# Performance work log

Hardware: AMD Instinct MI355X
Metric: run time of the kernel (lower is better)

## Reference

```python
import jax, jax.numpy as jnp
import numpy as np

DIM = 256
HEADS = 8
KS = 3          # deform conv kernel size
N = KS * KS     # sampling points per output pixel
PAD = 1


def conv2d(x, w, b=None, stride=1, padding=0):
    out = jax.lax.conv_general_dilated(
        x, w, (stride, stride), [(padding, padding)] * 2,
        dimension_numbers=('NCHW', 'OIHW', 'NCHW'))
    if b is not None:
        out = out + b[None, :, None, None]
    return out


def deform_conv(x, w_pconv, b_pconv, w_dconv):
    b, c, h, w = x.shape
    offset = conv2d(x, w_pconv, b_pconv, padding=1)      # (b, 2N, h, w)
    off = offset.transpose(0, 2, 3, 1)                   # (b, h, w, 2N); [:N]=x-off, [N:]=y-off
    xp = jnp.pad(x, ((0, 0), (0, 0), (PAD, PAD), (PAD, PAD)))
    hp, wp = h + 2 * PAD, w + 2 * PAD
    r = jnp.arange(-(KS - 1) // 2, (KS - 1) // 2 + 1, dtype=x.dtype)
    pnx, pny = jnp.meshgrid(r, r, indexing='ij')
    # sampling positions, 1-indexed into the padded input (matches the torch ref)
    px = off[..., :N] + pnx.reshape(-1) + jnp.arange(1, h + 1, dtype=x.dtype)[None, :, None, None]
    py = off[..., N:] + pny.reshape(-1) + jnp.arange(1, w + 1, dtype=x.dtype)[None, None, :, None]
    fx = jnp.floor(px)
    fy = jnp.floor(py)
    qlt_x = jnp.clip(fx, 0, hp - 1)
    qlt_y = jnp.clip(fy, 0, wp - 1)
    qrb_x = jnp.clip(fx + 1, 0, hp - 1)
    qrb_y = jnp.clip(fy + 1, 0, wp - 1)
    pxc = jnp.clip(px, 0, hp - 1)
    pyc = jnp.clip(py, 0, wp - 1)
    # bilinear weights (can be negative at clamped borders, as in the torch ref)
    g_lt = (1 + (qlt_x - pxc)) * (1 + (qlt_y - pyc))
    g_rb = (1 - (qrb_x - pxc)) * (1 - (qrb_y - pyc))
    g_lb = (1 + (qlt_x - pxc)) * (1 - (qrb_y - pyc))
    g_rt = (1 - (qrb_x - pxc)) * (1 + (qlt_y - pyc))
    ilt_x = qlt_x.astype(jnp.int32)
    ilt_y = qlt_y.astype(jnp.int32)
    irb_x = qrb_x.astype(jnp.int32)
    irb_y = qrb_y.astype(jnp.int32)

    def gather(xb, ix, iy):
        return xb[:, ix, iy]                              # (c, h, w, N)

    gat = jax.vmap(gather)
    x_lt = gat(xp, ilt_x, ilt_y)
    x_rb = gat(xp, irb_x, irb_y)
    x_lb = gat(xp, ilt_x, irb_y)
    x_rt = gat(xp, irb_x, ilt_y)
    x_off = (g_lt[:, None] * x_lt + g_rb[:, None] * x_rb
             + g_lb[:, None] * x_lb + g_rt[:, None] * x_rt)   # (b, c, h, w, N)
    # 'b c h w (i j) -> b c (h i) (w j)' then ks-strided conv
    x_off = x_off.reshape(b, c, h, w, KS, KS).transpose(0, 1, 2, 4, 3, 5)
    x_off = x_off.reshape(b, c, h * KS, w * KS)
    return conv2d(x_off, w_dconv, None, stride=KS)


def ssa_forward(x, w_pconv, b_pconv, w_dconv, w_qkv, temperature, w_proj):
    b, c, h, w = x.shape
    hw = h * w
    ch = c // HEADS
    q = deform_conv(x, w_pconv, b_pconv, w_dconv)         # (b, c, h, w)
    qkv = jnp.einsum('bchw,oc->bohw', x, w_qkv)           # 1x1 conv, (b, 3c, h, w)
    k = qkv[:, c:2 * c]
    v = qkv[:, 2 * c:]
    q = q.reshape(b, HEADS, ch, hw)
    k = k.reshape(b, HEADS, ch, hw)
    v = v.reshape(b, HEADS, ch, hw)
    k = k / jnp.maximum(jnp.linalg.norm(k, axis=-1, keepdims=True), 1e-12)
    v = v / jnp.maximum(jnp.linalg.norm(v, axis=-1, keepdims=True), 1e-12)
    attn = jnp.einsum('bhcn,bhdn->bhcd', q, k) * temperature[None]   # (b, h, ch, ch)
    attn = jax.nn.softmax(attn, axis=-1)
    out = jnp.einsum('bhcd,bhdn->bhcn', attn, v).reshape(b, c, h, w)
    return jnp.einsum('bchw,oc->bohw', out, w_proj)       # project_out 1x1


def setup_inputs() -> dict:
    key = jax.random.key(0)
    ks = jax.random.split(key, 6)
    B, H, W = 2, 96, 96
    x = jax.random.normal(ks[0], (B, DIM, H, W), jnp.float32)
    w_pconv = jax.random.normal(ks[1], (2 * N, DIM, KS, KS), jnp.float32) * 0.01
    b_pconv = jax.random.normal(ks[2], (2 * N,), jnp.float32) * 0.01
    w_dconv = jax.random.normal(ks[3], (DIM, DIM, KS, KS), jnp.float32) * 0.02
    w_qkv = jax.random.normal(ks[4], (3 * DIM, DIM), jnp.float32) * 0.05
    temperature = jnp.ones((HEADS, 1, 1), jnp.float32)
    w_proj = jax.random.normal(ks[5], (DIM, DIM), jnp.float32) * 0.05
    return dict(x=x, w_pconv=w_pconv, b_pconv=b_pconv, w_dconv=w_dconv,
                w_qkv=w_qkv, temperature=temperature, w_proj=w_proj)


def reference(x, w_pconv, b_pconv, w_dconv, w_qkv, temperature, w_proj):
    return ssa_forward(x, w_pconv, b_pconv, w_dconv, w_qkv, temperature, w_proj)
```

## Files before the change

### kernel.cpp

```cpp
#include <hip/hip_runtime.h>
#include <math.h>

#define BB 2
#define CC 256
#define HW 96
#define PP 9216
#define KO 18
#define HEADS 8
#define NCH 36

typedef short bf16x8 __attribute__((ext_vector_type(8)));
typedef float f32x4 __attribute__((ext_vector_type(4)));

#define NP_O    0UL
#define IDX_O   331776UL
#define WGT_O   995328UL
#define WT2_O   1658880UL
#define WP2_O   2248704UL
#define WQ2_O   2322432UL
#define W2_O    2453504UL
#define QP_O    2584576UL
#define KV_O    12021760UL
#define INV_O   21458944UL
#define AP_O    21459968UL
#define AT_O    22049792UL

__device__ __forceinline__ ushort f2bf_rne(float f) {
    unsigned u = __float_as_uint(f);
    unsigned r = (u + 0x7FFFu + ((u >> 16) & 1u)) >> 16;
    return (ushort)r;
}
__device__ __forceinline__ float bf2f(ushort h) {
    return __uint_as_float(((unsigned)h) << 16);
}

__global__ __launch_bounds__(256) void k_prep_wt(const float* __restrict__ wd,
                                                 ushort* __restrict__ h,
                                                 ushort* __restrict__ lo) {
    int tid = blockIdx.x * 256 + threadIdx.x;
    if (tid >= 9 * 8 * 1024 * 8) return;
    int e = tid & 7;
    int u = (tid >> 3) & 1023;
    int cs = (tid >> 13) & 7;
    int kk = tid >> 16;
    int oh = u >> 6, rem = u & 63;
    int lrow = rem & 15, lhi = rem >> 4;
    int o = oh * 16 + lrow;
    int c = cs * 32 + lhi * 8 + e;
    float v = wd[o * 2304 + c * 9 + kk];
    ushort hh = f2bf_rne(v);
    h[tid] = hh;
    lo[tid] = f2bf_rne(v - bf2f(hh));
}

__global__ __launch_bounds__(256) void k_prep_wp(const float* __restrict__ wp,
                                                 ushort* __restrict__ h,
                                                 ushort* __restrict__ lo) {
    int tid = blockIdx.x * 256 + threadIdx.x;
    if (tid >= 9 * 8 * 128 * 8) return;
    int e = tid & 7;
    int u = (tid >> 3) & 127;
    int cs = (tid >> 10) & 7;
    int kk = tid >> 13;
    int mf = u >> 6, rem = u & 63;
    int lrow = rem & 15, lhi = rem >> 4;
    int o = mf * 16 + lrow;
    int c = cs * 32 + lhi * 8 + e;
    float v = (o < KO) ? wp[(o * 256 + c) * 9 + kk] : 0.f;
    ushort hh = f2bf_rne(v);
    h[tid] = hh;
    lo[tid] = f2bf_rne(v - bf2f(hh));
}

__global__ __launch_bounds__(256) void k_prep_w(const float* __restrict__ W,
                                                ushort* __restrict__ h,
                                                ushort* __restrict__ lo,
                                                int total) {
    int tid = blockIdx.x * 256 + threadIdx.x;
    if (tid >= total) return;
    int e = tid & 7;
    int u = (tid >> 3) & 1023;
    int csg = (tid >> 13) & 7;
    int mt = tid >> 16;
    int rem = u & 63;
    int lrow = rem & 15, lhi = rem >> 4;
    int o = mt * 256 + (u >> 6) * 16 + lrow;
    int c = csg * 32 + lhi * 8 + e;
    float v = W[o * 256 + c];
    ushort hh = f2bf_rne(v);
    h[tid] = hh;
    lo[tid] = f2bf_rne(v - bf2f(hh));
}

__global__ __launch_bounds__(256) void k_pconv(const float* __restrict__ x,
                                               const ushort* __restrict__ wp2h,
                                               const ushort* __restrict__ wp2l,
                                               float* __restrict__ ppart) {
    int s = blockIdx.x;
    int xcd = s & 7;
    int b = xcd & 1, ks = xcd >> 1;
    int p0 = (s >> 3) * 64;
    int t = threadIdx.x;
    int l = t & 63, w = t >> 6;
    int lrow = l & 15, lhi = l >> 4;
    int p = t & 63, cg = t >> 6;
    __shared__ __align__(16) ushort Sh[64 * 40];
    __shared__ __align__(16) ushort Sl[64 * 40];
    f32x4 acc[2];
    acc[0] = (f32x4)0.f; acc[1] = (f32x4)0.f;
    const float* xb = x + (size_t)b * CC * PP;
    int pix = p0 + p;
    int i_ = pix / 96, j_ = pix % 96;
#pragma unroll 1
    for (int cs = 0; cs < 2; ++cs) {
        int csg = ks * 2 + cs;
        const float* xc0 = xb + (size_t)(csg * 32 + cg * 8) * PP;
#pragma unroll 1
        for (int kk = 0; kk < 9; ++kk) {
            int di = kk / 3 - 1, dj = kk % 3 - 1;
            bool vOK = ((unsigned)(i_ + di) < 96u) && ((unsigned)(j_ + dj) < 96u);
            int poff = pix + di * 96 + dj;
            __syncthreads();
            bf16x8 ah[2], al[2];
#pragma unroll
            for (int mf = 0; mf < 2; ++mf) {
                size_t gi = (((size_t)(kk * 8 + csg)) * 128 + (mf * 64 + l)) * 8;
                ah[mf] = *(const bf16x8*)&wp2h[gi];
                al[mf] = *(const bf16x8*)&wp2l[gi];
            }
            bf16x8 vh, vl;
#pragma unroll
            for (int i = 0; i < 8; ++i) {
                float v = vOK ? xc0[(size_t)i * PP + poff] : 0.f;
                ushort hh = f2bf_rne(v);
                vh[i] = (short)hh;
                vl[i] = (short)f2bf_rne(v - bf2f(hh));
            }
            *(bf16x8*)&Sh[p * 40 + cg * 8] = vh;
            *(bf16x8*)&Sl[p * 40 + cg * 8] = vl;
            __syncthreads();
            bf16x8 Bh = *(const bf16x8*)&Sh[(w * 16 + lrow) * 40 + lhi * 8];
            bf16x8 Bl = *(const bf16x8*)&Sl[(w * 16 + lrow) * 40 + lhi * 8];
#pragma unroll
            for (int mf = 0; mf < 2; ++mf) {
                acc[mf] = __builtin_amdgcn_mfma_f32_16x16x32_bf16(ah[mf], Bh, acc[mf], 0, 0, 0);
                acc[mf] = __builtin_amdgcn_mfma_f32_16x16x32_bf16(ah[mf], Bl, acc[mf], 0, 0, 0);
                acc[mf] = __builtin_amdgcn_mfma_f32_16x16x32_bf16(al[mf], Bh, acc[mf], 0, 0, 0);
            }
        }
    }
    float* pr = ppart + ((size_t)(ks * BB + b) * 32) * PP;
#pragma unroll
    for (int mf = 0; mf < 2; ++mf)
#pragma unroll
        for (int j = 0; j < 4; ++j)
            pr[(size_t)(mf * 16 + lhi * 4 + j) * PP + p0 + w * 16 + lrow] = acc[mf][j];
}

__global__ __launch_bounds__(256) void k_bilin2(const float* __restrict__ pp,
                                                const float* __restrict__ bp,
                                                int4* __restrict__ idx4,
                                                float4* __restrict__ wgt4) {
    int idx = blockIdx.x * 256 + threadIdx.x;
    if (idx >= BB * 9 * PP) return;
    int p = idx % PP;
    int bn = idx / PP;
    int n = bn % 9, b = bn / 9;
    int i = p / 96, j = p % 96;
    float ox = bp[n], oy = bp[n + 9];
#pragma unroll
    for (int k = 0; k < 4; ++k) {
        ox += pp[((size_t)(k * BB + b) * 32 + n) * PP + p];
        oy += pp[((size_t)(k * BB + b) * 32 + n + 9) * PP + p];
    }
    float px = ox + (float)(n / 3 - 1) + (float)(i + 1);
    float py = oy + (float)(n % 3 - 1) + (float)(j + 1);
    float fx = floorf(px), fy = floorf(py);
    float qltx = fminf(fmaxf(fx, 0.f), 97.f);
    float qlty = fminf(fmaxf(fy, 0.f), 97.f);
    float qrbx = fminf(fmaxf(fx + 1.f, 0.f), 97.f);
    float qrby = fminf(fmaxf(fy + 1.f, 0.f), 97.f);
    float pxc = fminf(fmaxf(px, 0.f), 97.f);
    float pyc = fminf(fmaxf(py, 0.f), 97.f);
    float glt = (1.f + (qltx - pxc)) * (1.f + (qlty - pyc));
    float grb = (1.f - (qrbx - pxc)) * (1.f - (qrby - pyc));
    float glb = (1.f + (qltx - pxc)) * (1.f - (qrby - pyc));
    float grt = (1.f - (qrbx - pxc)) * (1.f + (qlty - pyc));
    int x0 = (int)qltx - 1, y0 = (int)qlty - 1;
    int x1 = (int)qrbx - 1, y1 = (int)qrby - 1;
    bool vlt = (x0 >= 0 && x0 < 96 && y0 >= 0 && y0 < 96);
    bool vrb = (x1 >= 0 && x1 < 96 && y1 >= 0 && y1 < 96);
    bool vlb = (x0 >= 0 && x0 < 96 && y1 >= 0 && y1 < 96);
    bool vrt = (x1 >= 0 && x1 < 96 && y0 >= 0 && y0 < 96);
    int4 id;
    id.x = vlt ? x0 * 96 + y0 : 0;
    id.y = vrb ? x1 * 96 + y1 : 0;
    id.z = vlb ? x0 * 96 + y1 : 0;
    id.w = vrt ? x1 * 96 + y0 : 0;
    idx4[idx] = id;
    wgt4[idx] = make_float4(vlt ? glt : 0.f, vrb ? grb : 0.f,
                            vlb ? glb : 0.f, vrt ? grt : 0.f);
}

__global__ __launch_bounds__(256) void k_dconv(const float* __restrict__ x,
                                               const ushort* __restrict__ wt2h,
                                               const ushort* __restrict__ wt2l,
                                               const int4* __restrict__ idx4,
                                               const float4* __restrict__ wgt4,
                                               float* __restrict__ qpart) {
    int s = blockIdx.x;
    int xcd = s & 7, ib = s >> 3;
    int combo = xcd >> 1;
    int b = combo & 1;
    int half = combo >> 1;
    int ptile = (xcd & 1) * 144 + ib;
    int p0 = ptile * 32;
    int t = threadIdx.x;
    int l = t & 63, w = t >> 6;
    int lrow = l & 15, lhi = l >> 4;
    int obase = w * 64;
    int pl = t & 31, cg = t >> 5;

    __shared__ __align__(16) ushort Sh0[32 * 40], Sl0[32 * 40];
    __shared__ __align__(16) ushort Sh1[32 * 40], Sl1[32 * 40];
    __shared__ int4 Tid[9 * 32];
    __shared__ float4 Twg[9 * 32];

    for (int e = t; e < 9 * 32; e += 256) {
        int kk = e >> 5, pq = e & 31;
        size_t tb = ((size_t)b * 9 + kk) * PP + p0 + pq;
        Tid[e] = idx4[tb];
        Twg[e] = wgt4[tb];
    }

    f32x4 acc[4][2];
#pragma unroll
    for (int mf = 0; mf < 4; ++mf)
#pragma unroll
        for (int nf = 0; nf < 2; ++nf) acc[mf][nf] = (f32x4)0.f;

    const float* xb = x + (size_t)b * CC * PP;
    int h4 = half * 4;

    float R[16];
    float4 g4r;

    auto LD = [&](int i) {
        int cs = i / 9, kk = i % 9;
        int csg = h4 + cs;
        int4 id = Tid[kk * 32 + pl];
        g4r = Twg[kk * 32 + pl];
        const float* xp0 = xb + (size_t)(csg * 32 + cg * 4) * PP;
#pragma unroll
        for (int q = 0; q < 4; ++q) {
            const float* xc = xp0 + (size_t)q * PP;
            R[q * 4 + 0] = xc[id.x];
            R[q * 4 + 1] = xc[id.y];
            R[q * 4 + 2] = xc[id.z];
            R[q * 4 + 3] = xc[id.w];
        }
    };
    auto CONV = [&](ushort* Sh, ushort* Sl) {
        ushort4 vh, vl;
#pragma unroll
        for (int q = 0; q < 4; ++q) {
            float v = g4r.x * R[q * 4 + 0];
            v = fmaf(g4r.y, R[q * 4 + 1], v);
            v = fmaf(g4r.z, R[q * 4 + 2], v);
            v = fmaf(g4r.w, R[q * 4 + 3], v);
            ushort hh = f2bf_rne(v);
            ushort ll = f2bf_rne(v - bf2f(hh));
            if (q == 0)      { vh.x = hh; vl.x = ll; }
            else if (q == 1) { vh.y = hh; vl.y = ll; }
            else if (q == 2) { vh.z = hh; vl.z = ll; }
            else             { vh.w = hh; vl.w = ll; }
        }
        *(ushort4*)&Sh[pl * 40 + cg * 4] = vh;
        *(ushort4*)&Sl[pl * 40 + cg * 4] = vl;
    };
    auto COMPUTE = [&](int i, const ushort* Sh, const ushort* Sl) {
        int cs = i / 9, kk = i % 9;
        int csg = h4 + cs;
        bf16x8 ah[4], al[4];
#pragma unroll
        for (int mf = 0; mf < 4; ++mf) {
            size_t gi = (((size_t)(kk * 8 + csg)) * 1024 + ((w * 4 + mf) * 64 + l)) * 8;
            ah[mf] = *(const bf16x8*)&wt2h[gi];
            al[mf] = *(const bf16x8*)&wt2l[gi];
        }
        bf16x8 Bh2[2], Bl2[2];
#pragma unroll
        for (int nf = 0; nf < 2; ++nf) {
            Bh2[nf] = *(const bf16x8*)&Sh[(nf * 16 + lrow) * 40 + lhi * 8];
            Bl2[nf] = *(const bf16x8*)&Sl[(nf * 16 + lrow) * 40 + lhi * 8];
        }
        __builtin_amdgcn_s_setprio(1);
#pragma unroll
        for (int mf = 0; mf < 4; ++mf)
#pragma unroll
            for (int nf = 0; nf < 2; ++nf) {
                acc[mf][nf] = __builtin_amdgcn_mfma_f32_16x16x32_bf16(ah[mf], Bh2[nf], acc[mf][nf], 0, 0, 0);
                acc[mf][nf] = __builtin_amdgcn_mfma_f32_16x16x32_bf16(ah[mf], Bl2[nf], acc[mf][nf], 0, 0, 0);
                acc[mf][nf] = __builtin_amdgcn_mfma_f32_16x16x32_bf16(al[mf], Bh2[nf], acc[mf][nf], 0, 0, 0);
            }
        __builtin_amdgcn_s_setprio(0);
    };

    __syncthreads();
    LD(0); CONV(Sh0, Sl0);
    LD(1);
    __syncthreads();

#pragma unroll 1
    for (int i0 = 0; i0 < 36; i0 += 2) {
        CONV(Sh1, Sl1);
        if (i0 + 2 < 36) LD(i0 + 2);
        COMPUTE(i0, Sh0, Sl0);
        __syncthreads();
        if (i0 + 2 < 36) CONV(Sh0, Sl0);
        if (i0 + 3 < 36) LD(i0 + 3);
        COMPUTE(i0 + 1, Sh1, Sl1);
        __syncthreads();
    }

    float* qh = qpart + (size_t)half * BB * CC * PP + (size_t)b * CC * PP;
#pragma unroll
    for (int mf = 0; mf < 4; ++mf)
#pragma unroll
        for (int nf = 0; nf < 2; ++nf)
#pragma unroll
            for (int j = 0; j < 4; ++j)
                qh[(size_t)(obase + mf * 16 + lhi * 4 + j) * PP + p0 + nf * 16 + lrow] =
                    acc[mf][nf][j];
}

__global__ __launch_bounds__(256) void k_gemm_bf(const float* __restrict__ Bsrc,
                                                 const ushort* __restrict__ A2h,
                                                 const ushort* __restrict__ A2l,
                                                 float* __restrict__ C,
                                                 int mtiles, int bRowStride, int bRowOff,
                                                 int aBatchStride,
                                                 float* __restrict__ npart) {
    int s = blockIdx.x;
    int xcd = s & 7, ib = s >> 3;
    int b, mt, ptile;
    if (mtiles == 2) {
        int combo = xcd >> 1;
        b = combo & 1; mt = combo >> 1;
        ptile = (xcd & 1) * 72 + ib;
    } else {
        b = xcd >> 2; mt = 0;
        ptile = (xcd & 3) * 36 + ib;
    }
    int p0 = ptile * 64;
    int t = threadIdx.x;
    int l = t & 63, w = t >> 6;
    int lrow = l & 15, lhi = l >> 4;
    int obase = w * 64;
    int p = t & 63, cg = t >> 6;
    __shared__ __align__(16) ushort Sh[64 * 40];
    __shared__ __align__(16) ushort Sl[64 * 40];
    f32x4 acc[4][4];
#pragma unroll
    for (int mf = 0; mf < 4; ++mf)
#pragma unroll
        for (int nf = 0; nf < 4; ++nf) acc[mf][nf] = (f32x4)0.f;
    const float* Bb = Bsrc + ((size_t)b * bRowStride + bRowOff) * PP;
    const ushort* Ah = A2h + (size_t)b * aBatchStride;
    const ushort* Al = A2l + (size_t)b * aBatchStride;
#pragma unroll 1
    for (int csg = 0; csg < 8; ++csg) {
        __syncthreads();
        bf16x8 ah[4], al[4];
#pragma unroll
        for (int mf = 0; mf < 4; ++mf) {
            size_t gi = (((size_t)(mt * 8 + csg)) * 1024 + ((w * 4 + mf) * 64 + l)) * 8;
            ah[mf] = *(const bf16x8*)&Ah[gi];
            al[mf] = *(const bf16x8*)&Al[gi];
        }
        const float* xr = Bb + (size_t)(csg * 32 + cg * 8) * PP + p0 + p;
        bf16x8 vh, vl;
#pragma unroll
        for (int i = 0; i < 8; ++i) {
            float v = xr[(size_t)i * PP];
            ushort hh = f2bf_rne(v);
            vh[i] = (short)hh;
            vl[i] = (short)f2bf_rne(v - bf2f(hh));
        }
        *(bf16x8*)&Sh[p * 40 + cg * 8] = vh;
        *(bf16x8*)&Sl[p * 40 + cg * 8] = vl;
        __syncthreads();
        bf16x8 Bh4[4], Bl4[4];
#pragma unroll
        for (int nf = 0; nf < 4; ++nf) {
            Bh4[nf] = *(const bf16x8*)&Sh[(nf * 16 + lrow) * 40 + lhi * 8];
            Bl4[nf] = *(const bf16x8*)&Sl[(nf * 16 + lrow) * 40 + lhi * 8];
        }
#pragma unroll
        for (int mf = 0; mf < 4; ++mf) {
#pragma unroll
            for (int nf = 0; nf < 4; ++nf) {
                acc[mf][nf] = __builtin_amdgcn_mfma_f32_16x16x32_bf16(ah[mf], Bh4[nf], acc[mf][nf], 0, 0, 0);
                acc[mf][nf] = __builtin_amdgcn_mfma_f32_16x16x32_bf16(ah[mf], Bl4[nf], acc[mf][nf], 0, 0, 0);
                acc[mf][nf] = __builtin_amdgcn_mfma_f32_16x16x32_bf16(al[mf], Bh4[nf], acc[mf][nf], 0, 0, 0);
            }
        }
    }
    float* Cb = C + (size_t)b * (mtiles * 256) * PP;
#pragma unroll
    for (int mf = 0; mf < 4; ++mf)
#pragma unroll
        for (int nf = 0; nf < 4; ++nf)
#pragma unroll
            for (int j = 0; j < 4; ++j)
                Cb[(size_t)(mt * 256 + obase + mf * 16 + lhi * 4 + j) * PP + p0 + nf * 16 + lrow] =
                    acc[mf][nf][j];
    if (npart) {
        float sq[4][4];
#pragma unroll
        for (int mf = 0; mf < 4; ++mf)
#pragma unroll
            for (int j = 0; j < 4; ++j) {
                float v0 = acc[mf][0][j], v1 = acc[mf][1][j];
                float v2 = acc[mf][2][j], v3 = acc[mf][3][j];
                sq[mf][j] = v0 * v0 + v1 * v1 + v2 * v2 + v3 * v3;
            }
#pragma unroll
        for (int m = 1; m <= 8; m <<= 1)
#pragma unroll
            for (int mf = 0; mf < 4; ++mf)
#pragma unroll
                for (int j = 0; j < 4; ++j)
                    sq[mf][j] += __shfl_xor(sq[mf][j], m, 64);
        if (lrow == 0) {
            float* np = npart + ((size_t)(b * 2 + mt) * 144 + ptile) * 256;
#pragma unroll
            for (int mf = 0; mf < 4; ++mf)
#pragma unroll
                for (int j = 0; j < 4; ++j)
                    np[obase + mf * 16 + lhi * 4 + j] = sq[mf][j];
        }
    }
}

__global__ __launch_bounds__(256) void k_norm2(const float* __restrict__ np,
                                               float* __restrict__ invn) {
    int r = blockIdx.x * 256 + threadIdx.x;
    if (r >= 1024) return;
    int b = r >> 9, g = r & 511;
    int mt = g >> 8, row = g & 255;
    const float* base = np + ((size_t)(b * 2 + mt) * 144) * 256 + row;
    float s = 0.f;
    for (int pt = 0; pt < 144; ++pt) s += base[pt * 256];
    invn[b * 512 + g] = 1.f / fmaxf(sqrtf(s), 1e-12f);
}

__global__ __launch_bounds__(256) void k_attn_part(const float* __restrict__ qp,
                                                   const float* __restrict__ kv,
                                                   float* __restrict__ apart) {
    int ch = blockIdx.x, h = blockIdx.y, b = blockIdx.z;
    int t = threadIdx.x;
    int d = t & 31, cg = t >> 5;
    __shared__ float qs[32][37], ks[32][37];
    float acc[4] = {0.f, 0.f, 0.f, 0.f};
    const float* q0 = qp + ((size_t)b * CC + h * 32) * PP;
    const float* q1 = q0 + (size_t)BB * CC * PP;
    const float* kb = kv + ((size_t)b * 512 + h * 32) * PP;
    int r = t >> 3, cq = (t & 7) * 4;
    for (int po = ch * 256; po < ch * 256 + 256; po += 32) {
        float4 va = *(const float4*)&q0[(size_t)r * PP + po + cq];
        float4 vb = *(const float4*)&q1[(size_t)r * PP + po + cq];
        qs[r][cq + 0] = va.x + vb.x; qs[r][cq + 1] = va.y + vb.y;
        qs[r][cq + 2] = va.z + vb.z; qs[r][cq + 3] = va.w + vb.w;
        float4 vk = *(const float4*)&kb[(size_t)r * PP + po + cq];
        ks[r][cq + 0] = vk.x; ks[r][cq + 1] = vk.y;
        ks[r][cq + 2] = vk.z; ks[r][cq + 3] = vk.w;
        __syncthreads();
#pragma unroll
        for (int pq = 0; pq < 32; ++pq) {
            float kvv = ks[d][pq];
#pragma unroll
            for (int i = 0; i < 4; ++i)
                acc[i] = fmaf(qs[cg * 4 + i][pq], kvv, acc[i]);
        }
        __syncthreads();
    }
    float* ap = apart + (((size_t)(b * 8 + h) * NCH + ch) << 10);
#pragma unroll
    for (int i = 0; i < 4; ++i) ap[(cg * 4 + i) * 32 + d] = acc[i];
}

__global__ __launch_bounds__(256) void k_attn_fin(const float* __restrict__ apart,
                                                  const float* __restrict__ invn,
                                                  const float* __restrict__ temp,
                                                  float* __restrict__ attns) {
    int h = blockIdx.x, b = blockIdx.y;
    int t = threadIdx.x;
    __shared__ float A[32][33];
    const float* ap = apart + ((size_t)(b * 8 + h) * NCH << 10);
    float th = temp[h];
    for (int e = t; e < 1024; e += 256) {
        float s = 0.f;
        for (int chn = 0; chn < NCH; ++chn) s += ap[chn * 1024 + e];
        int c = e >> 5, d = e & 31;
        A[c][d] = s * th * invn[b * 512 + h * 32 + d];
    }
    __syncthreads();
    if (t < 32) {
        int c = t;
        float m = -INFINITY;
#pragma unroll
        for (int d = 0; d < 32; ++d) m = fmaxf(m, A[c][d]);
        float sum = 0.f;
#pragma unroll
        for (int d = 0; d < 32; ++d) sum += expf(A[c][d] - m);
        float inv = 1.f / sum;
        float* at = attns + ((size_t)(b * 8 + h) << 10) + c * 32;
#pragma unroll
        for (int d = 0; d < 32; ++d)
            at[d] = expf(A[c][d] - m) * inv * invn[b * 512 + 256 + h * 32 + d];
    }
}

__global__ __launch_bounds__(256) void k_w2(const float* __restrict__ attns,
                                            const float* __restrict__ wproj,
                                            ushort* __restrict__ w2h,
                                            ushort* __restrict__ w2l) {
    int h = blockIdx.x, b = blockIdx.y;
    int t = threadIdx.x;
    __shared__ float As[32][33];
    for (int e = t; e < 1024; e += 256)
        As[e >> 5][e & 31] = attns[((size_t)(b * 8 + h) << 10) + e];
    __syncthreads();
    int o = t;
    float wrow[32];
#pragma unroll
    for (int c = 0; c < 32; ++c) wrow[c] = wproj[o * 256 + h * 32 + c];
    int wq = o >> 6, mf = (o >> 4) & 3, lr = o & 15;
    size_t bb = (size_t)b * 65536;
#pragma unroll
    for (int e = 0; e < 32; ++e) {
        float v = 0.f;
#pragma unroll
        for (int c = 0; c < 32; ++c) v = fmaf(wrow[c], As[c][e], v);
        int lhi = e >> 3, ee = e & 7;
        size_t gi = bb + ((size_t)h * 1024 + ((wq * 4 + mf) * 64 + lhi * 16 + lr)) * 8 + ee;
        ushort hh = f2bf_rne(v);
        w2h[gi] = hh;
        w2l[gi] = f2bf_rne(v - bf2f(hh));
    }
}

extern "C" void kernel_launch(void* const* d_in, const int* in_sizes, int n_in,
                              void* d_out, int out_size, void* d_ws, size_t ws_size,
                              hipStream_t stream) {
    const float* x     = (const float*)d_in[0];
    const float* wp    = (const float*)d_in[1];
    const float* bp    = (const float*)d_in[2];
    const float* wd    = (const float*)d_in[3];
    const float* wqkv  = (const float*)d_in[4];
    const float* temp  = (const float*)d_in[5];
    const float* wproj = (const float*)d_in[6];
    float* out = (float*)d_out;
    float* ws  = (float*)d_ws;

    float* npart  = ws + NP_O;
    int4*  idx4   = (int4*)(ws + IDX_O);
    float4* wgt4  = (float4*)(ws + WGT_O);
    ushort* wt2h  = (ushort*)(ws + WT2_O);
    ushort* wt2l  = wt2h + 9 * 8 * 1024 * 8;
    ushort* wp2h  = (ushort*)(ws + WP2_O);
    ushort* wp2l  = wp2h + 9 * 8 * 128 * 8;
    ushort* wq2h  = (ushort*)(ws + WQ2_O);
    ushort* wq2l  = wq2h + 2 * 8 * 1024 * 8;
    ushort* w2h   = (ushort*)(ws + W2_O);
    ushort* w2l   = w2h + 2 * 65536;
    float* qpart  = ws + QP_O;
    float* ppart  = ws + QP_O;
    float* kv     = ws + KV_O;
    float* invn   = ws + INV_O;
    float* apart  = ws + AP_O;
    float* attns  = ws + AT_O;

    k_prep_wt<<<2304, 256, 0, stream>>>(wd, wt2h, wt2l);
    k_prep_wp<<<288, 256, 0, stream>>>(wp, wp2h, wp2l);
    k_prep_w<<<512, 256, 0, stream>>>(wqkv + 256 * 256, wq2h, wq2l, 2 * 65536);
    k_pconv<<<1152, 256, 0, stream>>>(x, wp2h, wp2l, ppart);
    k_bilin2<<<(BB * 9 * PP + 255) / 256, 256, 0, stream>>>(ppart, bp, idx4, wgt4);
    k_dconv<<<1152, 256, 0, stream>>>(x, wt2h, wt2l, idx4, wgt4, qpart);
    k_gemm_bf<<<576, 256, 0, stream>>>(x, wq2h, wq2l, kv, 2, 256, 0, 0, npart);
    k_norm2<<<4, 256, 0, stream>>>(npart, invn);
    k_attn_part<<<dim3(NCH, HEADS, BB), 256, 0, stream>>>(qpart, kv, apart);
    k_attn_fin<<<dim3(HEADS, BB), 256, 0, stream>>>(apart, invn, temp, attns);
    k_w2<<<dim3(HEADS, BB), 256, 0, stream>>>(attns, wproj, w2h, w2l);
    k_gemm_bf<<<288, 256, 0, stream>>>(kv, w2h, w2l, out, 1, 512, 256, 65536, nullptr);
}
```

Before: 299.5 us.

## Stage deform-conv weight tiles in LDS via direct loads, use 512-thread blocks

The deform-conv kernel now runs 512 threads per block. Each wave computes a 64x16 output sub-tile instead of 64x32. The per-step weight slice (hi and lo bf16) is copied into shared memory with global_load_lds direct loads, where before each wave read it from global memory with its own vector loads. The gather/convert work is also split so each thread handles 2 channels instead of 4, roughly halving the register footprint. The cost is a single-buffered weight tile with two barriers per step, so the weight load for step i no longer overlaps the MFMA work of the previous step.

```diff
diff --git a/kernel.cpp b/kernel.cpp
--- a/kernel.cpp
+++ b/kernel.cpp
@@ -32,6 +32,10 @@
 }
 __device__ __forceinline__ float bf2f(ushort h) {
     return __uint_as_float(((unsigned)h) << 16);
+}
+__device__ __forceinline__ void gload_lds16(const void* g, void* l) {
+    __builtin_amdgcn_global_load_lds((const __attribute__((address_space(1))) void*)g,
+                                     (__attribute__((address_space(3))) void*)l, 16, 0, 0);
 }
 
 __global__ __launch_bounds__(256) void k_prep_wt(const float* __restrict__ wd,
@@ -202,7 +206,7 @@
                             vlb ? glb : 0.f, vrt ? grt : 0.f);
 }
 
-__global__ __launch_bounds__(256) void k_dconv(const float* __restrict__ x,
+__global__ __launch_bounds__(512) void k_dconv(const float* __restrict__ x,
                                                const ushort* __restrict__ wt2h,
                                                const ushort* __restrict__ wt2l,
                                                const int4* __restrict__ idx4,
@@ -218,41 +222,54 @@
     int t = threadIdx.x;
     int l = t & 63, w = t >> 6;
     int lrow = l & 15, lhi = l >> 4;
-    int obase = w * 64;
-    int pl = t & 31, cg = t >> 5;
-
+    int mq = w >> 1, nh = w & 1;
+    int pl = t & 31, cgrp = t >> 5;
+
+    __shared__ __align__(16) ushort Ah_l[8192], Al_l[8192];
     __shared__ __align__(16) ushort Sh0[32 * 40], Sl0[32 * 40];
     __shared__ __align__(16) ushort Sh1[32 * 40], Sl1[32 * 40];
     __shared__ int4 Tid[9 * 32];
     __shared__ float4 Twg[9 * 32];
 
-    for (int e = t; e < 9 * 32; e += 256) {
+    for (int e = t; e < 9 * 32; e += 512) {
         int kk = e >> 5, pq = e & 31;
         size_t tb = ((size_t)b * 9 + kk) * PP + p0 + pq;
         Tid[e] = idx4[tb];
         Twg[e] = wgt4[tb];
     }
 
-    f32x4 acc[4][2];
-#pragma unroll
-    for (int mf = 0; mf < 4; ++mf)
-#pragma unroll
-        for (int nf = 0; nf < 2; ++nf) acc[mf][nf] = (f32x4)0.f;
+    f32x4 acc[4];
+#pragma unroll
+    for (int mf = 0; mf < 4; ++mf) acc[mf] = (f32x4)0.f;
 
     const float* xb = x + (size_t)b * CC * PP;
     int h4 = half * 4;
 
-    float R[16];
+    float R[8];
     float4 g4r;
 
+    auto ISSUE_A = [&](int i) {
+        int csg = h4 + i / 9, kk = i % 9;
+        const ushort* gh = wt2h + ((size_t)(kk * 8 + csg)) * 8192;
+        const ushort* gl = wt2l + ((size_t)(kk * 8 + csg)) * 8192;
+#pragma unroll
+        for (int r = 0; r < 2; ++r) {
+            int u = r * 512 + t;
+            gload_lds16(gh + (size_t)u * 8, &Ah_l[u * 8]);
+        }
+#pragma unroll
+        for (int r = 0; r < 2; ++r) {
+            int u = r * 512 + t;
+            gload_lds16(gl + (size_t)u * 8, &Al_l[u * 8]);
+        }
+    };
     auto LD = [&](int i) {
-        int cs = i / 9, kk = i % 9;
-        int csg = h4 + cs;
+        int csg = h4 + i / 9, kk = i % 9;
         int4 id = Tid[kk * 32 + pl];
         g4r = Twg[kk * 32 + pl];
-        const float* xp0 = xb + (size_t)(csg * 32 + cg * 4) * PP;
-#pragma unroll
-        for (int q = 0; q < 4; ++q) {
+        const float* xp0 = xb + (size_t)(csg * 32 + cgrp * 2) * PP;
+#pragma unroll
+        for (int q = 0; q < 2; ++q) {
             const float* xc = xp0 + (size_t)q * PP;
             R[q * 4 + 0] = xc[id.x];
             R[q * 4 + 1] = xc[id.y];
@@ -261,65 +278,51 @@
         }
     };
     auto CONV = [&](ushort* Sh, ushort* Sl) {
-        ushort4 vh, vl;
-#pragma unroll
-        for (int q = 0; q < 4; ++q) {
+        ushort2 vh, vl;
+#pragma unroll
+        for (int q = 0; q < 2; ++q) {
             float v = g4r.x * R[q * 4 + 0];
             v = fmaf(g4r.y, R[q * 4 + 1], v);
             v = fmaf(g4r.z, R[q * 4 + 2], v);
             v = fmaf(g4r.w, R[q * 4 + 3], v);
             ushort hh = f2bf_rne(v);
             ushort ll = f2bf_rne(v - bf2f(hh));
-            if (q == 0)      { vh.x = hh; vl.x = ll; }
-            else if (q == 1) { vh.y = hh; vl.y = ll; }
-            else if (q == 2) { vh.z = hh; vl.z = ll; }
-            else             { vh.w = hh; vl.w = ll; }
-        }
-        *(ushort4*)&Sh[pl * 40 + cg * 4] = vh;
-        *(ushort4*)&Sl[pl * 40 + cg * 4] = vl;
+            if (q == 0) { vh.x = hh; vl.x = ll; }
+            else        { vh.y = hh; vl.y = ll; }
+        }
+        *(ushort2*)&Sh[pl * 40 + cgrp * 2] = vh;
+        *(ushort2*)&Sl[pl * 40 + cgrp * 2] = vl;
     };
-    auto COMPUTE = [&](int i, const ushort* Sh, const ushort* Sl) {
-        int cs = i / 9, kk = i % 9;
-        int csg = h4 + cs;
+    auto COMPUTE = [&](const ushort* Sh, const ushort* Sl) {
         bf16x8 ah[4], al[4];
 #pragma unroll
         for (int mf = 0; mf < 4; ++mf) {
-            size_t gi = (((size_t)(kk * 8 + csg)) * 1024 + ((w * 4 + mf) * 64 + l)) * 8;
-            ah[mf] = *(const bf16x8*)&wt2h[gi];
-            al[mf] = *(const bf16x8*)&wt2l[gi];
-        }
-        bf16x8 Bh2[2], Bl2[2];
-#pragma unroll
-        for (int nf = 0; nf < 2; ++nf) {
-            Bh2[nf] = *(const bf16x8*)&Sh[(nf * 16 + lrow) * 40 + lhi * 8];
-            Bl2[nf] = *(const bf16x8*)&Sl[(nf * 16 + lrow) * 40 + lhi * 8];
-        }
+            ah[mf] = *(const bf16x8*)&Ah_l[((mq * 4 + mf) * 64 + l) * 8];
+            al[mf] = *(const bf16x8*)&Al_l[((mq * 4 + mf) * 64 + l) * 8];
+        }
+        bf16x8 Bh = *(const bf16x8*)&Sh[(nh * 16 + lrow) * 40 + lhi * 8];
+        bf16x8 Bl = *(const bf16x8*)&Sl[(nh * 16 + lrow) * 40 + lhi * 8];
         __builtin_amdgcn_s_setprio(1);
 #pragma unroll
-        for (int mf = 0; mf < 4; ++mf)
-#pragma unroll
-            for (int nf = 0; nf < 2; ++nf) {
-                acc[mf][nf] = __builtin_amdgcn_mfma_f32_16x16x32_bf16(ah[mf], Bh2[nf], acc[mf][nf], 0, 0, 0);
-                acc[mf][nf] = __builtin_amdgcn_mfma_f32_16x16x32_bf16(ah[mf], Bl2[nf], acc[mf][nf], 0, 0, 0);
-                acc[mf][nf] = __builtin_amdgcn_mfma_f32_16x16x32_bf16(al[mf], Bh2[nf], acc[mf][nf], 0, 0, 0);
-            }
+        for (int mf = 0; mf < 4; ++mf) {
+            acc[mf] = __builtin_amdgcn_mfma_f32_16x16x32_bf16(ah[mf], Bh, acc[mf], 0, 0, 0);
+            acc[mf] = __builtin_amdgcn_mfma_f32_16x16x32_bf16(ah[mf], Bl, acc[mf], 0, 0, 0);
+            acc[mf] = __builtin_amdgcn_mfma_f32_16x16x32_bf16(al[mf], Bh, acc[mf], 0, 0, 0);
+        }
         __builtin_amdgcn_s_setprio(0);
     };
 
     __syncthreads();
     LD(0); CONV(Sh0, Sl0);
     LD(1);
-    __syncthreads();
 
 #pragma unroll 1
-    for (int i0 = 0; i0 < 36; i0 += 2) {
-        CONV(Sh1, Sl1);
-        if (i0 + 2 < 36) LD(i0 + 2);
-        COMPUTE(i0, Sh0, Sl0);
+    for (int i = 0; i < 36; ++i) {
+        ISSUE_A(i);
+        if (i + 1 < 36) CONV((i & 1) ? Sh0 : Sh1, (i & 1) ? Sl0 : Sl1);
+        if (i + 2 < 36) LD(i + 2);
         __syncthreads();
-        if (i0 + 2 < 36) CONV(Sh0, Sl0);
-        if (i0 + 3 < 36) LD(i0 + 3);
-        COMPUTE(i0 + 1, Sh1, Sl1);
+        COMPUTE((i & 1) ? Sh1 : Sh0, (i & 1) ? Sl1 : Sl0);
         __syncthreads();
     }
 
@@ -327,11 +330,9 @@
 #pragma unroll
     for (int mf = 0; mf < 4; ++mf)
 #pragma unroll
-        for (int nf = 0; nf < 2; ++nf)
-#pragma unroll
-            for (int j = 0; j < 4; ++j)
-                qh[(size_t)(obase + mf * 16 + lhi * 4 + j) * PP + p0 + nf * 16 + lrow] =
-                    acc[mf][nf][j];
+        for (int j = 0; j < 4; ++j)
+            qh[(size_t)(mq * 64 + mf * 16 + lhi * 4 + j) * PP + p0 + nh * 16 + lrow] =
+                acc[mf][j];
 }
 
 __global__ __launch_bounds__(256) void k_gemm_bf(const float* __restrict__ Bsrc,
@@ -587,7 +588,7 @@
     k_prep_w<<<512, 256, 0, stream>>>(wqkv + 256 * 256, wq2h, wq2l, 2 * 65536);
     k_pconv<<<1152, 256, 0, stream>>>(x, wp2h, wp2l, ppart);
     k_bilin2<<<(BB * 9 * PP + 255) / 256, 256, 0, stream>>>(ppart, bp, idx4, wgt4);
-    k_dconv<<<1152, 256, 0, stream>>>(x, wt2h, wt2l, idx4, wgt4, qpart);
+    k_dconv<<<1152, 512, 0, stream>>>(x, wt2h, wt2l, idx4, wgt4, qpart);
     k_gemm_bf<<<576, 256, 0, stream>>>(x, wq2h, wq2l, kv, 2, 256, 0, 0, npart);
     k_norm2<<<4, 256, 0, stream>>>(npart, invn);
     k_attn_part<<<dim3(NCH, HEADS, BB), 256, 0, stream>>>(qpart, kv, apart);
```

New measurement: 321.1 us. 7.2% more time.

## Fuse norm/softmax/w2 kernels, pre-split V to bf16, halve attention partial chunks

Applied to the files above, without the earlier changes.

Merges the norm reduction, softmax and W2 projection kernels into one kernel, which removes two launches and the intermediate attention buffer. Adds a separate kernel that converts V into pre-tiled hi/lo bf16 pairs, so the final GEMM loads packed bf16 tiles instead of converting fp32 inline. Halves the number of attention-partial chunks, giving each block more work and leaving fewer partials to reduce. The extra prep kernel adds a full read/write pass over V in exchange for a cheaper GEMM load, and the workspace layout is reshuffled to fit the new buffers.

```diff
diff --git a/kernel.cpp b/kernel.cpp
--- a/kernel.cpp
+++ b/kernel.cpp
@@ -7,23 +7,23 @@
 #define PP 9216
 #define KO 18
 #define HEADS 8
-#define NCH 36
+#define NCH 18
 
 typedef short bf16x8 __attribute__((ext_vector_type(8)));
 typedef float f32x4 __attribute__((ext_vector_type(4)));
 
 #define NP_O    0UL
+#define W2_O    147456UL
 #define IDX_O   331776UL
 #define WGT_O   995328UL
 #define WT2_O   1658880UL
 #define WP2_O   2248704UL
 #define WQ2_O   2322432UL
-#define W2_O    2453504UL
 #define QP_O    2584576UL
 #define KV_O    12021760UL
 #define INV_O   21458944UL
 #define AP_O    21459968UL
-#define AT_O    22049792UL
+#define V2T_O   331776UL
 
 __device__ __forceinline__ ushort f2bf_rne(float f) {
     unsigned u = __float_as_uint(f);
@@ -335,6 +335,8 @@
 }
 
 __global__ __launch_bounds__(256) void k_gemm_bf(const float* __restrict__ Bsrc,
+                                                 const ushort* __restrict__ B2h,
+                                                 const ushort* __restrict__ B2l,
                                                  const ushort* __restrict__ A2h,
                                                  const ushort* __restrict__ A2l,
                                                  float* __restrict__ C,
@@ -365,7 +367,6 @@
     for (int mf = 0; mf < 4; ++mf)
 #pragma unroll
         for (int nf = 0; nf < 4; ++nf) acc[mf][nf] = (f32x4)0.f;
-    const float* Bb = Bsrc + ((size_t)b * bRowStride + bRowOff) * PP;
     const ushort* Ah = A2h + (size_t)b * aBatchStride;
     const ushort* Al = A2l + (size_t)b * aBatchStride;
 #pragma unroll 1
@@ -378,17 +379,26 @@
             ah[mf] = *(const bf16x8*)&Ah[gi];
             al[mf] = *(const bf16x8*)&Al[gi];
         }
-        const float* xr = Bb + (size_t)(csg * 32 + cg * 8) * PP + p0 + p;
-        bf16x8 vh, vl;
-#pragma unroll
-        for (int i = 0; i < 8; ++i) {
-            float v = xr[(size_t)i * PP];
-            ushort hh = f2bf_rne(v);
-            vh[i] = (short)hh;
-            vl[i] = (short)f2bf_rne(v - bf2f(hh));
-        }
-        *(bf16x8*)&Sh[p * 40 + cg * 8] = vh;
-        *(bf16x8*)&Sl[p * 40 + cg * 8] = vl;
+        if (B2h) {
+            size_t bo = ((((size_t)b * 144 + ptile) * 8 + csg) * 4 + cg) * 512 + (size_t)p * 8;
+            bf16x8 vh = *(const bf16x8*)&B2h[bo];
+            bf16x8 vl = *(const bf16x8*)&B2l[bo];
+            *(bf16x8*)&Sh[p * 40 + cg * 8] = vh;
+            *(bf16x8*)&Sl[p * 40 + cg * 8] = vl;
+        } else {
+            const float* Bb = Bsrc + ((size_t)b * bRowStride + bRowOff) * PP;
+            const float* xr = Bb + (size_t)(csg * 32 + cg * 8) * PP + p0 + p;
+            bf16x8 vh, vl;
+#pragma unroll
+            for (int i = 0; i < 8; ++i) {
+                float v = xr[(size_t)i * PP];
+                ushort hh = f2bf_rne(v);
+                vh[i] = (short)hh;
+                vl[i] = (short)f2bf_rne(v - bf2f(hh));
+            }
+            *(bf16x8*)&Sh[p * 40 + cg * 8] = vh;
+            *(bf16x8*)&Sl[p * 40 + cg * 8] = vl;
+        }
         __syncthreads();
         bf16x8 Bh4[4], Bl4[4];
 #pragma unroll
@@ -443,16 +453,37 @@
     }
 }
 
-__global__ __launch_bounds__(256) void k_norm2(const float* __restrict__ np,
-                                               float* __restrict__ invn) {
-    int r = blockIdx.x * 256 + threadIdx.x;
-    if (r >= 1024) return;
-    int b = r >> 9, g = r & 511;
-    int mt = g >> 8, row = g & 255;
-    const float* base = np + ((size_t)(b * 2 + mt) * 144) * 256 + row;
-    float s = 0.f;
-    for (int pt = 0; pt < 144; ++pt) s += base[pt * 256];
-    invn[b * 512 + g] = 1.f / fmaxf(sqrtf(s), 1e-12f);
+__global__ __launch_bounds__(256) void k_prep_v(const float* __restrict__ kv,
+                                                ushort* __restrict__ v2h,
+                                                ushort* __restrict__ v2l) {
+    int s = blockIdx.x;
+    int b = s / 1152;
+    int r = s % 1152;
+    int pt = r >> 3, csg = r & 7;
+    int t = threadIdx.x;
+    __shared__ float T[32][65];
+    const float* src = kv + ((size_t)b * 512 + 256 + csg * 32) * PP + pt * 64;
+    {
+        int c = t >> 3, p8 = (t & 7) * 8;
+        const float* row = src + (size_t)c * PP + p8;
+        float4 a = *(const float4*)&row[0];
+        float4 d = *(const float4*)&row[4];
+        T[c][p8 + 0] = a.x; T[c][p8 + 1] = a.y; T[c][p8 + 2] = a.z; T[c][p8 + 3] = a.w;
+        T[c][p8 + 4] = d.x; T[c][p8 + 5] = d.y; T[c][p8 + 6] = d.z; T[c][p8 + 7] = d.w;
+    }
+    __syncthreads();
+    int cc = t >> 6, pl = t & 63;
+    bf16x8 vh, vl;
+#pragma unroll
+    for (int e = 0; e < 8; ++e) {
+        float v = T[cc * 8 + e][pl];
+        ushort hh = f2bf_rne(v);
+        vh[e] = (short)hh;
+        vl[e] = (short)f2bf_rne(v - bf2f(hh));
+    }
+    size_t o = ((((size_t)b * 144 + pt) * 8 + csg) * 4 + cc) * 512 + (size_t)pl * 8;
+    *(bf16x8*)&v2h[o] = vh;
+    *(bf16x8*)&v2l[o] = vl;
 }
 
 __global__ __launch_bounds__(256) void k_attn_part(const float* __restrict__ qp,
@@ -467,7 +498,7 @@
     const float* q1 = q0 + (size_t)BB * CC * PP;
     const float* kb = kv + ((size_t)b * 512 + h * 32) * PP;
     int r = t >> 3, cq = (t & 7) * 4;
-    for (int po = ch * 256; po < ch * 256 + 256; po += 32) {
+    for (int po = ch * 512; po < ch * 512 + 512; po += 32) {
         float4 va = *(const float4*)&q0[(size_t)r * PP + po + cq];
         float4 vb = *(const float4*)&q1[(size_t)r * PP + po + cq];
         qs[r][cq + 0] = va.x + vb.x; qs[r][cq + 1] = va.y + vb.y;
@@ -490,47 +521,49 @@
     for (int i = 0; i < 4; ++i) ap[(cg * 4 + i) * 32 + d] = acc[i];
 }
 
-__global__ __launch_bounds__(256) void k_attn_fin(const float* __restrict__ apart,
-                                                  const float* __restrict__ invn,
-                                                  const float* __restrict__ temp,
-                                                  float* __restrict__ attns) {
+__global__ __launch_bounds__(256) void k_attn_fin_w2(const float* __restrict__ apart,
+                                                     const float* __restrict__ npart,
+                                                     const float* __restrict__ temp,
+                                                     const float* __restrict__ wproj,
+                                                     ushort* __restrict__ w2h,
+                                                     ushort* __restrict__ w2l) {
     int h = blockIdx.x, b = blockIdx.y;
     int t = threadIdx.x;
     __shared__ float A[32][33];
+    __shared__ float invk[32], invv[32];
+    if (t < 64) {
+        int mt = t >> 5, row = (t & 31) + h * 32;
+        const float* base = npart + ((size_t)(b * 2 + mt) * 144) * 256 + row;
+        float ssum = 0.f;
+        for (int pt = 0; pt < 144; ++pt) ssum += base[pt * 256];
+        float iv = 1.f / fmaxf(sqrtf(ssum), 1e-12f);
+        if (mt == 0) invk[t & 31] = iv; else invv[t & 31] = iv;
+    }
     const float* ap = apart + ((size_t)(b * 8 + h) * NCH << 10);
     float th = temp[h];
     for (int e = t; e < 1024; e += 256) {
         float s = 0.f;
         for (int chn = 0; chn < NCH; ++chn) s += ap[chn * 1024 + e];
-        int c = e >> 5, d = e & 31;
-        A[c][d] = s * th * invn[b * 512 + h * 32 + d];
+        A[e >> 5][e & 31] = s * th;
     }
     __syncthreads();
     if (t < 32) {
         int c = t;
         float m = -INFINITY;
-#pragma unroll
-        for (int d = 0; d < 32; ++d) m = fmaxf(m, A[c][d]);
+        float row[32];
+#pragma unroll
+        for (int d = 0; d < 32; ++d) {
+            row[d] = A[c][d] * invk[d];
+            m = fmaxf(m, row[d]);
+        }
         float sum = 0.f;
 #pragma unroll
-        for (int d = 0; d < 32; ++d) sum += expf(A[c][d] - m);
+        for (int d = 0; d < 32; ++d) sum += expf(row[d] - m);
         float inv = 1.f / sum;
-        float* at = attns + ((size_t)(b * 8 + h) << 10) + c * 32;
 #pragma unroll
         for (int d = 0; d < 32; ++d)
-            at[d] = expf(A[c][d] - m) * inv * invn[b * 512 + 256 + h * 32 + d];
-    }
-}
-
-__global__ __launch_bounds__(256) void k_w2(const float* __restrict__ attns,
-                                            const float* __restrict__ wproj,
-                                            ushort* __restrict__ w2h,
-                                            ushort* __restrict__ w2l) {
-    int h = blockIdx.x, b = blockIdx.y;
-    int t = threadIdx.x;
-    __shared__ float As[32][33];
-    for (int e = t; e < 1024; e += 256)
-        As[e >> 5][e & 31] = attns[((size_t)(b * 8 + h) << 10) + e];
+            A[c][d] = expf(row[d] - m) * inv * invv[d];
+    }
     __syncthreads();
     int o = t;
     float wrow[32];
@@ -542,7 +575,7 @@
     for (int e = 0; e < 32; ++e) {
         float v = 0.f;
 #pragma unroll
-        for (int c = 0; c < 32; ++c) v = fmaf(wrow[c], As[c][e], v);
+        for (int c = 0; c < 32; ++c) v = fmaf(wrow[c], A[c][e], v);
         int lhi = e >> 3, ee = e & 7;
         size_t gi = bb + ((size_t)h * 1024 + ((wq * 4 + mf) * 64 + lhi * 16 + lr)) * 8 + ee;
         ushort hh = f2bf_rne(v);
@@ -565,6 +598,8 @@
     float* ws  = (float*)d_ws;
 
     float* npart  = ws + NP_O;
+    ushort* w2h   = (ushort*)(ws + W2_O);
+    ushort* w2l   = w2h + 2 * 65536;
     int4*  idx4   = (int4*)(ws + IDX_O);
     float4* wgt4  = (float4*)(ws + WGT_O);
     ushort* wt2h  = (ushort*)(ws + WT2_O);
@@ -573,14 +608,12 @@
     ushort* wp2l  = wp2h + 9 * 8 * 128 * 8;
     ushort* wq2h  = (ushort*)(ws + WQ2_O);
     ushort* wq2l  = wq2h + 2 * 8 * 1024 * 8;
-    ushort* w2h   = (ushort*)(ws + W2_O);
-    ushort* w2l   = w2h + 2 * 65536;
     float* qpart  = ws + QP_O;
     float* ppart  = ws + QP_O;
     float* kv     = ws + KV_O;
-    float* invn   = ws + INV_O;
     float* apart  = ws + AP_O;
-    float* attns  = ws + AT_O;
+    ushort* v2th  = (ushort*)(ws + V2T_O);
+    ushort* v2tl  = v2th + 4718592;
 
     k_prep_wt<<<2304, 256, 0, stream>>>(wd, wt2h, wt2l);
     k_prep_wp<<<288, 256, 0, stream>>>(wp, wp2h, wp2l);
@@ -588,10 +621,11 @@
     k_pconv<<<1152, 256, 0, stream>>>(x, wp2h, wp2l, ppart);
     k_bilin2<<<(BB * 9 * PP + 255) / 256, 256, 0, stream>>>(ppart, bp, idx4, wgt4);
     k_dconv<<<1152, 256, 0, stream>>>(x, wt2h, wt2l, idx4, wgt4, qpart);
-    k_gemm_bf<<<576, 256, 0, stream>>>(x, wq2h, wq2l, kv, 2, 256, 0, 0, npart);
-    k_norm2<<<4, 256, 0, stream>>>(npart, invn);
+    k_gemm_bf<<<576, 256, 0, stream>>>(x, nullptr, nullptr, wq2h, wq2l, kv,
+                                       2, 256, 0, 0, npart);
     k_attn_part<<<dim3(NCH, HEADS, BB), 256, 0, stream>>>(qpart, kv, apart);
-    k_attn_fin<<<dim3(HEADS, BB), 256, 0, stream>>>(apart, invn, temp, attns);
-    k_w2<<<dim3(HEADS, BB), 256, 0, stream>>>(attns, wproj, w2h, w2l);
-    k_gemm_bf<<<288, 256, 0, stream>>>(kv, w2h, w2l, out, 1, 512, 256, 65536, nullptr);
-}
+    k_attn_fin_w2<<<dim3(HEADS, BB), 256, 0, stream>>>(apart, npart, temp, wproj, w2h, w2l);
+    k_prep_v<<<2304, 256, 0, stream>>>(kv, v2th, v2tl);
+    k_gemm_bf<<<288, 256, 0, stream>>>(nullptr, v2th, v2tl, w2h, w2l, out,
+                                       1, 0, 0, 65536, nullptr);
+}
```

Result: no change. 304.3 us (+1.6%).
